# Kernel tuning notes

Measured on AMD Instinct MI355X. Metric: run time of the kernel, lower is better.

Reference implementation:

```python
import jax, jax.numpy as jnp
import numpy as np

B, T, D, H, E, K = 4, 2048, 1024, 2048, 8, 2
LN_EPS = 1e-5


def setup_inputs() -> dict:
    key = jax.random.key(0)
    ks = jax.random.split(key, 5)
    sc = 0.02  # init scale for weights
    return {
        "x": jax.random.normal(ks[0], (B, T, D), dtype=jnp.float32),
        "gate_W": jax.random.normal(ks[1], (D, E), dtype=jnp.float32) * sc,
        "gate_b": jnp.zeros((E,), dtype=jnp.float32),
        "W1": jax.random.normal(ks[2], (E, D, H), dtype=jnp.float32) * sc,
        "b1": jnp.zeros((E, H), dtype=jnp.float32),
        "W2": jax.random.normal(ks[3], (E, H, D), dtype=jnp.float32) * sc,
        "b2": jnp.zeros((E, D), dtype=jnp.float32),
        "ln_gamma": jnp.ones((D,), dtype=jnp.float32),
        "ln_beta": jnp.zeros((D,), dtype=jnp.float32),
    }


def reference(x, gate_W, gate_b, W1, b1, W2, b2, ln_gamma, ln_beta):
    b, t, d = x.shape
    tokens = x.reshape(b * t, d)                      # [N, D]
    n = tokens.shape[0]

    # --- noisy top-k router (eval mode: no noise) ---
    logits = tokens @ gate_W + gate_b                 # [N, E]
    topk_val, topk_idx = jax.lax.top_k(logits, K)     # [N, K]
    topk_prob = jax.nn.softmax(topk_val, axis=-1)
    gates = jnp.zeros_like(logits).at[jnp.arange(n)[:, None], topk_idx].set(topk_prob)  # [N, E]

    # --- experts: dense-equivalent of gather-MLP-scatter (gates are 0 for unselected) ---
    h = jax.nn.gelu(jnp.einsum('nd,edh->enh', tokens, W1) + b1[:, None, :], approximate=False)  # [E,N,H]
    y = jnp.einsum('enh,ehd->end', h, W2) + b2[:, None, :]                                      # [E,N,D]
    out = jnp.einsum('ne,end->nd', gates, y).reshape(b, t, d)

    # --- residual + layernorm ---
    z = out + x
    mu = jnp.mean(z, axis=-1, keepdims=True)
    var = jnp.var(z, axis=-1, keepdims=True)
    out = (z - mu) * jax.lax.rsqrt(var + LN_EPS) * ln_gamma + ln_beta

    # --- aux losses ---
    route_probs = jax.nn.softmax(logits, axis=-1)     # [N, E]
    importance = route_probs.mean(axis=0)             # [E]
    load = (gates > 0).astype(jnp.float32).mean(axis=0)  # [E]
    balance_loss = E * jnp.sum(importance * load)
    eps = 1e-8
    entropy = -(route_probs * jnp.log(route_probs + eps)).sum(axis=-1).mean()
    utilization_entropy = -(load * jnp.log(load + eps)).sum()
    return out, balance_loss, entropy, utilization_entropy, load, importance
```

## Files before the change

### kernel.cpp

```cpp
#include <hip/hip_runtime.h>
#include <math.h>

#define N_TOK 8192
#define DIM   1024
#define HID   2048
#define NE    8
#define NPAIR (N_TOK * 2)
#define CAPP  (NPAIR + NE * 128)
#define TAIL  (N_TOK * DIM)

typedef __bf16 bf16x8_t __attribute__((ext_vector_type(8)));
typedef float  f32x4_t  __attribute__((ext_vector_type(4)));

__device__ __forceinline__ unsigned short f2bf(float f) {
  union { float f; unsigned u; } v; v.f = f;
  unsigned r = v.u + 0x7fffu + ((v.u >> 16) & 1u);
  return (unsigned short)(r >> 16);
}

__device__ __forceinline__ float bf2f(unsigned short h) {
  union { unsigned u; float f; } v; v.u = ((unsigned)h) << 16;
  return v.f;
}

__device__ __forceinline__ float gelu_exact(float v) {
  return 0.5f * v * (1.f + erff(v * 0.70710678118654752440f));
}

__device__ __forceinline__ void load16_lds(const void* g, void* l) {
  __builtin_amdgcn_global_load_lds(
      (const __attribute__((address_space(1))) unsigned int*)g,
      (__attribute__((address_space(3))) unsigned int*)l, 16, 0, 0);
}


template<int KD, int RR>
__global__ __launch_bounds__(256) void w_to_frag(const float* __restrict__ src,
                                                 unsigned short* __restrict__ dst) {
  constexpr int KD32 = KD / 32;
  int z = blockIdx.z;
  int cl = blockIdx.x * 4 + (threadIdx.x >> 6);
  int lane = threadIdx.x & 63, m16 = lane & 15, q = lane >> 4;
  int rblk = cl / KD32, kblk = cl % KD32;
  int r = rblk * 16 + m16;
  int kb = kblk * 32 + q * 8;
  const float* s = src + (size_t)z * KD * RR + (size_t)kb * RR + r;
  unsigned short t[8];
  #pragma unroll
  for (int j = 0; j < 8; ++j) t[j] = f2bf(s[(size_t)j * RR]);
  *(uint4*)(dst + (size_t)z * KD * RR + (size_t)cl * 512 + lane * 8) = *(uint4*)t;
}

#define R_BLOCKS 128
#define R_TPW    (N_TOK / (R_BLOCKS * 4))
__global__ __launch_bounds__(256) void router_kernel(
    const float* __restrict__ x, const float* __restrict__ gW, const float* __restrict__ gb,
    int* __restrict__ tok_e, float* __restrict__ tok_g,
    int* __restrict__ cnt, float* __restrict__ imp, float* __restrict__ ent_sum) {
  __shared__ int s_cnt[NE];
  __shared__ float s_imp[NE];
  __shared__ float s_ent;
  int tid = threadIdx.x;
  if (tid < NE) { s_cnt[tid] = 0; s_imp[tid] = 0.f; }
  if (tid == 0) s_ent = 0.f;
  __syncthreads();
  int wid = tid >> 6, lane = tid & 63;
  int t0 = (blockIdx.x * 4 + wid) * R_TPW;
  float imp_loc[8] = {0.f, 0.f, 0.f, 0.f, 0.f, 0.f, 0.f, 0.f};
  float ent_loc = 0.f;
  for (int t = 0; t < R_TPW; ++t) {
    int n = t0 + t;
    const float* xr = x + (size_t)n * DIM;
    float p[8] = {0.f, 0.f, 0.f, 0.f, 0.f, 0.f, 0.f, 0.f};
    #pragma unroll
    for (int it = 0; it < DIM / 64; ++it) {
      int d = lane + (it << 6);
      float xv = xr[d];
      const float4* g4 = (const float4*)(gW + (size_t)d * NE);
      float4 a = g4[0], b = g4[1];
      p[0] += xv * a.x; p[1] += xv * a.y; p[2] += xv * a.z; p[3] += xv * a.w;
      p[4] += xv * b.x; p[5] += xv * b.y; p[6] += xv * b.z; p[7] += xv * b.w;
    }
    #pragma unroll
    for (int e = 0; e < 8; ++e)
      for (int o = 32; o > 0; o >>= 1) p[e] += __shfl_down(p[e], o, 64);
    if (lane == 0) {
      float lg[8];
      #pragma unroll
      for (int e = 0; e < 8; ++e) lg[e] = p[e] + gb[e];
      int i0 = 0;
      #pragma unroll
      for (int e = 1; e < 8; ++e) if (lg[e] > lg[i0]) i0 = e;
      int i1 = (i0 == 0) ? 1 : 0;
      #pragma unroll
      for (int e = 0; e < 8; ++e) if (e != i0 && lg[e] > lg[i1]) i1 = e;
      float d1 = expf(lg[i1] - lg[i0]);
      float g0 = 1.f / (1.f + d1);
      float g1 = d1 * g0;
      tok_e[2 * n] = i0; tok_e[2 * n + 1] = i1;
      tok_g[2 * n] = g0; tok_g[2 * n + 1] = g1;
      atomicAdd(&s_cnt[i0], 1);
      atomicAdd(&s_cnt[i1], 1);
      float mx = lg[i0], s = 0.f, pe[8];
      #pragma unroll
      for (int e = 0; e < 8; ++e) { pe[e] = expf(lg[e] - mx); s += pe[e]; }
      float inv = 1.f / s;
      #pragma unroll
      for (int e = 0; e < 8; ++e) {
        float pr = pe[e] * inv;
        imp_loc[e] += pr;
        ent_loc -= pr * logf(pr + 1e-8f);
      }
    }
  }
  if (lane == 0) {
    #pragma unroll
    for (int e = 0; e < 8; ++e) atomicAdd(&s_imp[e], imp_loc[e]);
    atomicAdd(&s_ent, ent_loc);
  }
  __syncthreads();
  const float invN = 1.f / (float)N_TOK;
  if (tid < NE) {
    atomicAdd(&cnt[tid], s_cnt[tid]);
    atomicAdd(&imp[tid], s_imp[tid] * invN);
  }
  if (tid == NE) atomicAdd(ent_sum, s_ent * invN);
}

__global__ void finalize_kernel(const int* __restrict__ cnt, int* __restrict__ poffs,
                                int* __restrict__ cursor, const float* __restrict__ imp,
                                const float* __restrict__ ent_sum, float* __restrict__ out_tail) {
  if (threadIdx.x == 0) {
    int off = 0; float bal = 0.f, util = 0.f;
    for (int e = 0; e < NE; ++e) {
      poffs[e] = off; cursor[e] = off;
      off += ((cnt[e] + 127) >> 7) << 7;
      float ld = (float)cnt[e] * (1.f / (float)N_TOK);
      float im = imp[e];
      out_tail[3 + e] = ld;
      out_tail[11 + e] = im;
      bal += im * ld;
      util -= ld * logf(ld + 1e-8f);
    }
    poffs[NE] = off;
    out_tail[0] = (float)NE * bal;
    out_tail[1] = *ent_sum;
    out_tail[2] = util;
  }
}

__global__ __launch_bounds__(256) void scatter_kernel(
    const int* __restrict__ tok_e, const float* __restrict__ tok_g,
    int* __restrict__ cursor, int* __restrict__ row_token, float* __restrict__ row_gate,
    int* __restrict__ pair_slot) {
  __shared__ int s_cnt[NE], s_base[NE], s_rank[NE];
  int tid = threadIdx.x;
  if (tid < NE) { s_cnt[tid] = 0; s_rank[tid] = 0; }
  __syncthreads();
  int n = blockIdx.x * 256 + tid;
  int e0 = tok_e[2 * n], e1 = tok_e[2 * n + 1];
  atomicAdd(&s_cnt[e0], 1);
  atomicAdd(&s_cnt[e1], 1);
  __syncthreads();
  if (tid < NE) s_base[tid] = atomicAdd(&cursor[tid], s_cnt[tid]);
  __syncthreads();
  int r0 = atomicAdd(&s_rank[e0], 1);
  int s0 = s_base[e0] + r0;
  row_token[s0] = n; row_gate[s0] = tok_g[2 * n]; pair_slot[2 * n] = s0;
  int r1 = atomicAdd(&s_rank[e1], 1);
  int s1 = s_base[e1] + r1;
  row_token[s1] = n; row_gate[s1] = tok_g[2 * n + 1]; pair_slot[2 * n + 1] = s1;
}

__global__ __launch_bounds__(256) void gather_a1(
    const float* __restrict__ x, const int* __restrict__ row_token,
    const int* __restrict__ cnt, const int* __restrict__ poffs,
    unsigned short* __restrict__ Ab1) {
  int e = blockIdx.z;
  int base = poffs[e];
  int pcnt = poffs[e + 1] - base;
  int nch = (pcnt >> 4) * 32;
  int cl = blockIdx.x * 4 + (threadIdx.x >> 6);
  if (cl >= nch) return;
  int lane = threadIdx.x & 63, m16 = lane & 15, q = lane >> 4;
  int rblk = cl >> 5, kblk = cl & 31;
  int sl = rblk * 16 + m16;
  int slot = base + sl;
  int tok = (sl < cnt[e]) ? row_token[slot] : 0;
  int k = kblk * 32 + q * 8;
  const float4* sp = (const float4*)(x + (size_t)tok * DIM + k);
  float4 v0 = sp[0], v1 = sp[1];
  unsigned short t[8] = {f2bf(v0.x), f2bf(v0.y), f2bf(v0.z), f2bf(v0.w),
                         f2bf(v1.x), f2bf(v1.y), f2bf(v1.z), f2bf(v1.w)};
  *(uint4*)(Ab1 + ((size_t)(slot >> 4) * 32 + kblk) * 512 + lane * 8) = *(uint4*)t;
}

__global__ __launch_bounds__(256, 4) void expert_gemm1(
    const unsigned short* __restrict__ Ab1,
    const unsigned short* __restrict__ W1f,
    const float* __restrict__ b1,
    const int* __restrict__ poffs,
    unsigned short* __restrict__ He) {
  __shared__ __align__(16) unsigned short As[8192], Bs[8192];
  int e = blockIdx.z;
  int base = poffs[e];
  int pcnt = poffs[e + 1] - base;
  int row0 = blockIdx.x * 128;
  if (row0 >= pcnt) return;
  int col0 = blockIdx.y * 128;
  int tid = threadIdx.x, wid = tid >> 6, lane = tid & 63;
  int m16 = lane & 15, q = lane >> 4;
  int wr = (wid & 1) << 6, wc = (wid >> 1) << 6;
  const unsigned short* Ag = Ab1 + ((size_t)(((base + row0) >> 4) + wid * 2) * 32) * 512 + lane * 8;
  const unsigned short* Bg = W1f + (size_t)e * HID * DIM
                           + ((size_t)((col0 >> 4) + wid * 2) * 32) * 512 + lane * 8;
  unsigned short* lA = As + wid * 4 * 512;
  unsigned short* lB = Bs + wid * 4 * 512;
  f32x4_t zero4 = {0.f, 0.f, 0.f, 0.f};
  f32x4_t acc[4][4];
  #pragma unroll
  for (int i = 0; i < 4; ++i)
    #pragma unroll
    for (int j = 0; j < 4; ++j) acc[i][j] = zero4;
  int ra = wr >> 4, rc = wc >> 4;
  for (int k0 = 0; k0 < DIM; k0 += 64) {
    int kc = (k0 >> 5) * 512;
    load16_lds(Ag + kc,                  lA);
    load16_lds(Ag + kc + 512,            lA + 512);
    load16_lds(Ag + kc + 32 * 512,       lA + 1024);
    load16_lds(Ag + kc + 32 * 512 + 512, lA + 1536);
    load16_lds(Bg + kc,                  lB);
    load16_lds(Bg + kc + 512,            lB + 512);
    load16_lds(Bg + kc + 32 * 512,       lB + 1024);
    load16_lds(Bg + kc + 32 * 512 + 512, lB + 1536);
    __syncthreads();
    #pragma unroll
    for (int ks = 0; ks < 2; ++ks) {
      bf16x8_t a[4], b[4];
      #pragma unroll
      for (int i = 0; i < 4; ++i) {
        a[i] = *(const bf16x8_t*)&As[((ra + i) * 2 + ks) * 512 + lane * 8];
        b[i] = *(const bf16x8_t*)&Bs[((rc + i) * 2 + ks) * 512 + lane * 8];
      }
      #pragma unroll
      for (int i = 0; i < 4; ++i)
        #pragma unroll
        for (int j = 0; j < 4; ++j)
          acc[i][j] = __builtin_amdgcn_mfma_f32_16x16x32_bf16(a[i], b[j], acc[i][j], 0, 0, 0);
    }
    __syncthreads();
  }
  const float* b1e = b1 + (size_t)e * HID;
  int sb = (base + row0) >> 4;
  #pragma unroll
  for (int i = 0; i < 4; ++i) {
    size_t sblk = (size_t)(sb + ra + i);
    #pragma unroll
    for (int rr = 0; rr < 4; ++rr) {
      int s15 = q * 4 + rr;
      #pragma unroll
      for (int j = 0; j < 4; ++j) {
        int col = col0 + wc + j * 16 + m16;
        float v = acc[i][j][rr] + b1e[col];
        size_t off = (sblk * 64 + (col >> 5)) * 512 + (((col >> 3) & 3) * 16 + s15) * 8 + (col & 7);
        He[off] = f2bf(gelu_exact(v));
      }
    }
  }
}

__global__ __launch_bounds__(256, 4) void expert_gemm2(
    const unsigned short* __restrict__ He,
    const unsigned short* __restrict__ W2f,
    const int* __restrict__ poffs,
    unsigned short* __restrict__ yb) {
  __shared__ __align__(16) unsigned short As[8192], Bs[8192];
  int e = blockIdx.z;
  int base = poffs[e];
  int pcnt = poffs[e + 1] - base;
  int row0 = blockIdx.x * 128;
  if (row0 >= pcnt) return;
  int col0 = blockIdx.y * 128;
  int tid = threadIdx.x, wid = tid >> 6, lane = tid & 63;
  int m16 = lane & 15, q = lane >> 4;
  int wr = (wid & 1) << 6, wc = (wid >> 1) << 6;
  const unsigned short* Ag = He + ((size_t)(((base + row0) >> 4) + wid * 2) * 64) * 512 + lane * 8;
  const unsigned short* Bg = W2f + (size_t)e * DIM * HID
                           + ((size_t)((col0 >> 4) + wid * 2) * 64) * 512 + lane * 8;
  unsigned short* lA = As + wid * 4 * 512;
  unsigned short* lB = Bs + wid * 4 * 512;
  f32x4_t zero4 = {0.f, 0.f, 0.f, 0.f};
  f32x4_t acc[4][4];
  #pragma unroll
  for (int i = 0; i < 4; ++i)
    #pragma unroll
    for (int j = 0; j < 4; ++j) acc[i][j] = zero4;
  int ra = wr >> 4, rc = wc >> 4;
  for (int k0 = 0; k0 < HID; k0 += 64) {
    int kc = (k0 >> 5) * 512;
    load16_lds(Ag + kc,                  lA);
    load16_lds(Ag + kc + 512,            lA + 512);
    load16_lds(Ag + kc + 64 * 512,       lA + 1024);
    load16_lds(Ag + kc + 64 * 512 + 512, lA + 1536);
    load16_lds(Bg + kc,                  lB);
    load16_lds(Bg + kc + 512,            lB + 512);
    load16_lds(Bg + kc + 64 * 512,       lB + 1024);
    load16_lds(Bg + kc + 64 * 512 + 512, lB + 1536);
    __syncthreads();
    #pragma unroll
    for (int ks = 0; ks < 2; ++ks) {
      bf16x8_t a[4], b[4];
      #pragma unroll
      for (int i = 0; i < 4; ++i) {
        a[i] = *(const bf16x8_t*)&As[((ra + i) * 2 + ks) * 512 + lane * 8];
        b[i] = *(const bf16x8_t*)&Bs[((rc + i) * 2 + ks) * 512 + lane * 8];
      }
      #pragma unroll
      for (int i = 0; i < 4; ++i)
        #pragma unroll
        for (int j = 0; j < 4; ++j)
          acc[i][j] = __builtin_amdgcn_mfma_f32_16x16x32_bf16(a[i], b[j], acc[i][j], 0, 0, 0);
    }
    __syncthreads();
  }
  #pragma unroll
  for (int i = 0; i < 4; ++i) {
    #pragma unroll
    for (int rr = 0; rr < 4; ++rr) {
      size_t slot = (size_t)(base + row0 + wr + i * 16 + q * 4 + rr);
      #pragma unroll
      for (int j = 0; j < 4; ++j) {
        int col = col0 + wc + j * 16 + m16;
        yb[slot * DIM + col] = f2bf(acc[i][j][rr]);
      }
    }
  }
}

__global__ __launch_bounds__(256) void ln_kernel(
    const float* __restrict__ x, const unsigned short* __restrict__ yb,
    const int* __restrict__ tok_e, const float* __restrict__ tok_g,
    const int* __restrict__ pair_slot, const float* __restrict__ b2,
    const float* __restrict__ gamma, const float* __restrict__ beta,
    float* __restrict__ out) {
  int n = blockIdx.x, tid = threadIdx.x;
  int e0 = tok_e[2 * n], e1 = tok_e[2 * n + 1];
  float g0 = tok_g[2 * n], g1 = tok_g[2 * n + 1];
  size_t s0 = (size_t)pair_slot[2 * n], s1 = (size_t)pair_slot[2 * n + 1];
  const float* xr = x + (size_t)n * DIM;
  const unsigned short* y0 = yb + s0 * DIM;
  const unsigned short* y1 = yb + s1 * DIM;
  const float* b2e0 = b2 + (size_t)e0 * DIM;
  const float* b2e1 = b2 + (size_t)e1 * DIM;
  float z[4], s = 0.f, s2 = 0.f;
  #pragma unroll
  for (int jj = 0; jj < 4; ++jj) {
    int d = tid + (jj << 8);
    float v = xr[d] + g0 * (bf2f(y0[d]) + b2e0[d]) + g1 * (bf2f(y1[d]) + b2e1[d]);
    z[jj] = v; s += v; s2 += v * v;
  }
  for (int o = 32; o > 0; o >>= 1) { s += __shfl_down(s, o, 64); s2 += __shfl_down(s2, o, 64); }
  __shared__ float rs[4], rs2[4];
  int wid = tid >> 6, lane = tid & 63;
  if (lane == 0) { rs[wid] = s; rs2[wid] = s2; }
  __syncthreads();
  float ts = rs[0] + rs[1] + rs[2] + rs[3];
  float ts2 = rs2[0] + rs2[1] + rs2[2] + rs2[3];
  float mu = ts * (1.f / DIM);
  float var = ts2 * (1.f / DIM) - mu * mu;
  float rstd = rsqrtf(var + 1e-5f);
  float* orow = out + (size_t)n * DIM;
  #pragma unroll
  for (int jj = 0; jj < 4; ++jj) {
    int d = tid + (jj << 8);
    orow[d] = (z[jj] - mu) * rstd * gamma[d] + beta[d];
  }
}

extern "C" void kernel_launch(void* const* d_in, const int* in_sizes, int n_in,
                              void* d_out, int out_size, void* d_ws, size_t ws_size,
                              hipStream_t stream) {
  const float* x     = (const float*)d_in[0];
  const float* gW    = (const float*)d_in[1];
  const float* gb    = (const float*)d_in[2];
  const float* W1    = (const float*)d_in[3];
  const float* b1    = (const float*)d_in[4];
  const float* W2    = (const float*)d_in[5];
  const float* b2    = (const float*)d_in[6];
  const float* gamma = (const float*)d_in[7];
  const float* beta  = (const float*)d_in[8];
  float* out = (float*)d_out;

  char* w = (char*)d_ws;
  unsigned short* W1f = (unsigned short*)w; w += (size_t)NE * HID * DIM * 2;
  unsigned short* W2f = (unsigned short*)w; w += (size_t)NE * DIM * HID * 2;
  unsigned short* He  = (unsigned short*)w; w += (size_t)CAPP * HID * 2;
  unsigned short* AbY = (unsigned short*)w; w += (size_t)CAPP * DIM * 2;
  int*   row_token    = (int*)w;            w += (size_t)CAPP * 4;
  float* row_gate     = (float*)w;          w += (size_t)CAPP * 4;
  int*   tok_e        = (int*)w;            w += (size_t)NPAIR * 4;
  float* tok_g        = (float*)w;          w += (size_t)NPAIR * 4;
  int*   pair_slot    = (int*)w;            w += (size_t)NPAIR * 4;
  float* imp          = (float*)w;
  float* ent_sum      = imp + 8;
  int*   cntp         = (int*)(imp + 16);
  int*   cursor       = cntp + 8;
  int*   poffs        = cursor + 8;

  unsigned short* Ab1 = AbY;
  unsigned short* yb  = AbY;

  hipMemsetAsync(imp, 0, 256, stream);

  w_to_frag<DIM, HID><<<dim3(1024, 1, NE), 256, 0, stream>>>(W1, W1f);
  w_to_frag<HID, DIM><<<dim3(1024, 1, NE), 256, 0, stream>>>(W2, W2f);
  router_kernel<<<R_BLOCKS, 256, 0, stream>>>(x, gW, gb, tok_e, tok_g, cntp, imp, ent_sum);
  finalize_kernel<<<1, 64, 0, stream>>>(cntp, poffs, cursor, imp, ent_sum, out + TAIL);
  scatter_kernel<<<N_TOK / 256, 256, 0, stream>>>(tok_e, tok_g, cursor, row_token, row_gate, pair_slot);
  gather_a1<<<dim3(4096, 1, NE), 256, 0, stream>>>(x, row_token, cntp, poffs, Ab1);
  expert_gemm1<<<dim3(64, HID / 128, NE), 256, 0, stream>>>(Ab1, W1f, b1, poffs, He);
  expert_gemm2<<<dim3(64, DIM / 128, NE), 256, 0, stream>>>(He, W2f, poffs, yb);
  ln_kernel<<<N_TOK, 256, 0, stream>>>(x, yb, tok_e, tok_g, pair_slot, b2, gamma, beta, out);
}
```

Measured before the change: 523.0 us.

## Use persistent work-queue tiles in expert GEMMs, fast erf GELU, staged He stores

Both expert GEMMs become persistent kernels that pull tiles from an atomic work counter, using per-expert tile prefix offsets computed in finalize. This avoids launching mostly-empty blocks for the worst-case grid of 64 row tiles per expert. The GEMM1 epilogue now stages GELU output through LDS and writes 16-byte vector stores into He. Exact erf is replaced by the Abramowitz–Stegun polynomial approximation with __expf, which adds a small accuracy error. The router block count is also raised.

```diff
diff --git a/kernel.cpp b/kernel.cpp
--- a/kernel.cpp
+++ b/kernel.cpp
@@ -23,8 +23,15 @@
   return v.f;
 }
 
-__device__ __forceinline__ float gelu_exact(float v) {
-  return 0.5f * v * (1.f + erff(v * 0.70710678118654752440f));
+__device__ __forceinline__ float gelu_fast(float v) {
+  float u = v * 0.70710678118654752440f;
+  float z = fabsf(u);
+  float t = 1.f / (1.f + 0.3275911f * z);
+  float poly = t * (0.254829592f + t * (-0.284496736f + t * (1.421413741f +
+               t * (-1.453152027f + t * 1.061405429f))));
+  float er = 1.f - poly * __expf(-z * z);
+  er = (u < 0.f) ? -er : er;
+  return 0.5f * v * (1.f + er);
 }
 
 __device__ __forceinline__ void load16_lds(const void* g, void* l) {
@@ -51,7 +58,7 @@
   *(uint4*)(dst + (size_t)z * KD * RR + (size_t)cl * 512 + lane * 8) = *(uint4*)t;
 }
 
-#define R_BLOCKS 128
+#define R_BLOCKS 512
 #define R_TPW    (N_TOK / (R_BLOCKS * 4))
 __global__ __launch_bounds__(256) void router_kernel(
     const float* __restrict__ x, const float* __restrict__ gW, const float* __restrict__ gb,
@@ -128,13 +135,18 @@
 }
 
 __global__ void finalize_kernel(const int* __restrict__ cnt, int* __restrict__ poffs,
-                                int* __restrict__ cursor, const float* __restrict__ imp,
+                                int* __restrict__ cursor, int* __restrict__ tb1,
+                                int* __restrict__ tb2, const float* __restrict__ imp,
                                 const float* __restrict__ ent_sum, float* __restrict__ out_tail) {
   if (threadIdx.x == 0) {
-    int off = 0; float bal = 0.f, util = 0.f;
+    int off = 0, t1 = 0, t2 = 0; float bal = 0.f, util = 0.f;
     for (int e = 0; e < NE; ++e) {
-      poffs[e] = off; cursor[e] = off;
-      off += ((cnt[e] + 127) >> 7) << 7;
+      poffs[e] = off; cursor[e] = off; tb1[e] = t1; tb2[e] = t2;
+      int pc = ((cnt[e] + 127) >> 7) << 7;
+      off += pc;
+      int nt = pc >> 7;
+      t1 += nt * (HID / 128);
+      t2 += nt * (DIM / 128);
       float ld = (float)cnt[e] * (1.f / (float)N_TOK);
       float im = imp[e];
       out_tail[3 + e] = ld;
@@ -142,7 +154,7 @@
       bal += im * ld;
       util -= ld * logf(ld + 1e-8f);
     }
-    poffs[NE] = off;
+    poffs[NE] = off; tb1[NE] = t1; tb2[NE] = t2;
     out_tail[0] = (float)NE * bal;
     out_tail[1] = *ent_sum;
     out_tail[2] = util;
@@ -199,141 +211,173 @@
     const unsigned short* __restrict__ Ab1,
     const unsigned short* __restrict__ W1f,
     const float* __restrict__ b1,
-    const int* __restrict__ poffs,
+    const int* __restrict__ poffs, const int* __restrict__ tb1,
+    int* __restrict__ wq,
     unsigned short* __restrict__ He) {
-  __shared__ __align__(16) unsigned short As[8192], Bs[8192];
-  int e = blockIdx.z;
-  int base = poffs[e];
-  int pcnt = poffs[e + 1] - base;
-  int row0 = blockIdx.x * 128;
-  if (row0 >= pcnt) return;
-  int col0 = blockIdx.y * 128;
-  int tid = threadIdx.x, wid = tid >> 6, lane = tid & 63;
+  __shared__ __align__(16) unsigned short Sm[16384];
+  __shared__ int s_tb[NE + 1], s_po[NE + 1], s_t;
+  int tid = threadIdx.x;
+  if (tid <= NE) { s_tb[tid] = tb1[tid]; s_po[tid] = poffs[tid]; }
+  int wid = tid >> 6, lane = tid & 63;
   int m16 = lane & 15, q = lane >> 4;
   int wr = (wid & 1) << 6, wc = (wid >> 1) << 6;
-  const unsigned short* Ag = Ab1 + ((size_t)(((base + row0) >> 4) + wid * 2) * 32) * 512 + lane * 8;
-  const unsigned short* Bg = W1f + (size_t)e * HID * DIM
-                           + ((size_t)((col0 >> 4) + wid * 2) * 32) * 512 + lane * 8;
-  unsigned short* lA = As + wid * 4 * 512;
-  unsigned short* lB = Bs + wid * 4 * 512;
-  f32x4_t zero4 = {0.f, 0.f, 0.f, 0.f};
-  f32x4_t acc[4][4];
-  #pragma unroll
-  for (int i = 0; i < 4; ++i)
-    #pragma unroll
-    for (int j = 0; j < 4; ++j) acc[i][j] = zero4;
   int ra = wr >> 4, rc = wc >> 4;
-  for (int k0 = 0; k0 < DIM; k0 += 64) {
-    int kc = (k0 >> 5) * 512;
-    load16_lds(Ag + kc,                  lA);
-    load16_lds(Ag + kc + 512,            lA + 512);
-    load16_lds(Ag + kc + 32 * 512,       lA + 1024);
-    load16_lds(Ag + kc + 32 * 512 + 512, lA + 1536);
-    load16_lds(Bg + kc,                  lB);
-    load16_lds(Bg + kc + 512,            lB + 512);
-    load16_lds(Bg + kc + 32 * 512,       lB + 1024);
-    load16_lds(Bg + kc + 32 * 512 + 512, lB + 1536);
+  unsigned short* As = Sm;
+  unsigned short* Bs = Sm + 8192;
+  unsigned short* lA = As + wid * 2048;
+  unsigned short* lB = Bs + wid * 2048;
+  unsigned short* Rg = Sm + wid * 4096;
+  for (;;) {
+    if (tid == 0) s_t = atomicAdd(wq, 1);
     __syncthreads();
-    #pragma unroll
-    for (int ks = 0; ks < 2; ++ks) {
-      bf16x8_t a[4], b[4];
-      #pragma unroll
-      for (int i = 0; i < 4; ++i) {
-        a[i] = *(const bf16x8_t*)&As[((ra + i) * 2 + ks) * 512 + lane * 8];
-        b[i] = *(const bf16x8_t*)&Bs[((rc + i) * 2 + ks) * 512 + lane * 8];
+    int t = s_t;
+    if (t >= s_tb[NE]) break;
+    int e = 0;
+    #pragma unroll
+    for (int k = 1; k < NE; ++k) e += (t >= s_tb[k]);
+    int lt = t - s_tb[e];
+    int rt = lt >> 4, ct = lt & 15;
+    int base = s_po[e];
+    int row0 = rt * 128, col0 = ct * 128;
+    const unsigned short* Ag = Ab1 + ((size_t)(((base + row0) >> 4) + wid * 2) * 32) * 512 + lane * 8;
+    const unsigned short* Bg = W1f + (size_t)e * (HID * DIM)
+                             + ((size_t)((col0 >> 4) + wid * 2) * 32) * 512 + lane * 8;
+    f32x4_t zero4 = {0.f, 0.f, 0.f, 0.f};
+    f32x4_t acc[4][4];
+    #pragma unroll
+    for (int i = 0; i < 4; ++i)
+      #pragma unroll
+      for (int j = 0; j < 4; ++j) acc[i][j] = zero4;
+    for (int k0 = 0; k0 < DIM; k0 += 64) {
+      int kc = (k0 >> 5) * 512;
+      load16_lds(Ag + kc,                  lA);
+      load16_lds(Ag + kc + 512,            lA + 512);
+      load16_lds(Ag + kc + 32 * 512,       lA + 1024);
+      load16_lds(Ag + kc + 32 * 512 + 512, lA + 1536);
+      load16_lds(Bg + kc,                  lB);
+      load16_lds(Bg + kc + 512,            lB + 512);
+      load16_lds(Bg + kc + 32 * 512,       lB + 1024);
+      load16_lds(Bg + kc + 32 * 512 + 512, lB + 1536);
+      __syncthreads();
+      #pragma unroll
+      for (int ks = 0; ks < 2; ++ks) {
+        bf16x8_t a[4], b[4];
+        #pragma unroll
+        for (int i = 0; i < 4; ++i) {
+          a[i] = *(const bf16x8_t*)&As[((ra + i) * 2 + ks) * 512 + lane * 8];
+          b[i] = *(const bf16x8_t*)&Bs[((rc + i) * 2 + ks) * 512 + lane * 8];
+        }
+        #pragma unroll
+        for (int i = 0; i < 4; ++i)
+          #pragma unroll
+          for (int j = 0; j < 4; ++j)
+            acc[i][j] = __builtin_amdgcn_mfma_f32_16x16x32_bf16(a[i], b[j], acc[i][j], 0, 0, 0);
       }
-      #pragma unroll
-      for (int i = 0; i < 4; ++i)
-        #pragma unroll
-        for (int j = 0; j < 4; ++j)
-          acc[i][j] = __builtin_amdgcn_mfma_f32_16x16x32_bf16(a[i], b[j], acc[i][j], 0, 0, 0);
+      __syncthreads();
+    }
+    const float* b1e = b1 + (size_t)e * HID;
+    float b1v[4];
+    #pragma unroll
+    for (int j = 0; j < 4; ++j) b1v[j] = b1e[col0 + wc + j * 16 + m16];
+    #pragma unroll
+    for (int i = 0; i < 4; ++i)
+      #pragma unroll
+      for (int j = 0; j < 4; ++j)
+        #pragma unroll
+        for (int rr = 0; rr < 4; ++rr) {
+          float v = acc[i][j][rr] + b1v[j];
+          Rg[(i * 2 + (j >> 1)) * 512 +
+             (((j & 1) * 2 + (m16 >> 3)) * 16 + q * 4 + rr) * 8 + (m16 & 7)] = f2bf(gelu_fast(v));
+        }
+    int sb0 = ((base + row0) >> 4) + ra;
+    int kg0 = (col0 >> 5) + (wc >> 5);
+    #pragma unroll
+    for (int c = 0; c < 8; ++c) {
+      size_t go = ((size_t)(sb0 + (c >> 1)) * 64 + kg0 + (c & 1)) * 512 + lane * 8;
+      *(uint4*)(He + go) = *(uint4*)&Rg[c * 512 + lane * 8];
     }
     __syncthreads();
-  }
-  const float* b1e = b1 + (size_t)e * HID;
-  int sb = (base + row0) >> 4;
-  #pragma unroll
-  for (int i = 0; i < 4; ++i) {
-    size_t sblk = (size_t)(sb + ra + i);
-    #pragma unroll
-    for (int rr = 0; rr < 4; ++rr) {
-      int s15 = q * 4 + rr;
-      #pragma unroll
-      for (int j = 0; j < 4; ++j) {
-        int col = col0 + wc + j * 16 + m16;
-        float v = acc[i][j][rr] + b1e[col];
-        size_t off = (sblk * 64 + (col >> 5)) * 512 + (((col >> 3) & 3) * 16 + s15) * 8 + (col & 7);
-        He[off] = f2bf(gelu_exact(v));
-      }
-    }
   }
 }
 
 __global__ __launch_bounds__(256, 4) void expert_gemm2(
     const unsigned short* __restrict__ He,
     const unsigned short* __restrict__ W2f,
-    const int* __restrict__ poffs,
+    const int* __restrict__ poffs, const int* __restrict__ tb2,
+    int* __restrict__ wq,
     unsigned short* __restrict__ yb) {
-  __shared__ __align__(16) unsigned short As[8192], Bs[8192];
-  int e = blockIdx.z;
-  int base = poffs[e];
-  int pcnt = poffs[e + 1] - base;
-  int row0 = blockIdx.x * 128;
-  if (row0 >= pcnt) return;
-  int col0 = blockIdx.y * 128;
-  int tid = threadIdx.x, wid = tid >> 6, lane = tid & 63;
+  __shared__ __align__(16) unsigned short Sm[16384];
+  __shared__ int s_tb[NE + 1], s_po[NE + 1], s_t;
+  int tid = threadIdx.x;
+  if (tid <= NE) { s_tb[tid] = tb2[tid]; s_po[tid] = poffs[tid]; }
+  int wid = tid >> 6, lane = tid & 63;
   int m16 = lane & 15, q = lane >> 4;
   int wr = (wid & 1) << 6, wc = (wid >> 1) << 6;
-  const unsigned short* Ag = He + ((size_t)(((base + row0) >> 4) + wid * 2) * 64) * 512 + lane * 8;
-  const unsigned short* Bg = W2f + (size_t)e * DIM * HID
-                           + ((size_t)((col0 >> 4) + wid * 2) * 64) * 512 + lane * 8;
-  unsigned short* lA = As + wid * 4 * 512;
-  unsigned short* lB = Bs + wid * 4 * 512;
-  f32x4_t zero4 = {0.f, 0.f, 0.f, 0.f};
-  f32x4_t acc[4][4];
-  #pragma unroll
-  for (int i = 0; i < 4; ++i)
-    #pragma unroll
-    for (int j = 0; j < 4; ++j) acc[i][j] = zero4;
   int ra = wr >> 4, rc = wc >> 4;
-  for (int k0 = 0; k0 < HID; k0 += 64) {
-    int kc = (k0 >> 5) * 512;
-    load16_lds(Ag + kc,                  lA);
-    load16_lds(Ag + kc + 512,            lA + 512);
-    load16_lds(Ag + kc + 64 * 512,       lA + 1024);
-    load16_lds(Ag + kc + 64 * 512 + 512, lA + 1536);
-    load16_lds(Bg + kc,                  lB);
-    load16_lds(Bg + kc + 512,            lB + 512);
-    load16_lds(Bg + kc + 64 * 512,       lB + 1024);
-    load16_lds(Bg + kc + 64 * 512 + 512, lB + 1536);
+  unsigned short* As = Sm;
+  unsigned short* Bs = Sm + 8192;
+  unsigned short* lA = As + wid * 2048;
+  unsigned short* lB = Bs + wid * 2048;
+  for (;;) {
+    if (tid == 0) s_t = atomicAdd(wq, 1);
     __syncthreads();
-    #pragma unroll
-    for (int ks = 0; ks < 2; ++ks) {
-      bf16x8_t a[4], b[4];
-      #pragma unroll
-      for (int i = 0; i < 4; ++i) {
-        a[i] = *(const bf16x8_t*)&As[((ra + i) * 2 + ks) * 512 + lane * 8];
-        b[i] = *(const bf16x8_t*)&Bs[((rc + i) * 2 + ks) * 512 + lane * 8];
+    int t = s_t;
+    if (t >= s_tb[NE]) break;
+    int e = 0;
+    #pragma unroll
+    for (int k = 1; k < NE; ++k) e += (t >= s_tb[k]);
+    int lt = t - s_tb[e];
+    int rt = lt >> 3, ct = lt & 7;
+    int base = s_po[e];
+    int row0 = rt * 128, col0 = ct * 128;
+    const unsigned short* Ag = He + ((size_t)(((base + row0) >> 4) + wid * 2) * 64) * 512 + lane * 8;
+    const unsigned short* Bg = W2f + (size_t)e * (DIM * HID)
+                             + ((size_t)((col0 >> 4) + wid * 2) * 64) * 512 + lane * 8;
+    f32x4_t zero4 = {0.f, 0.f, 0.f, 0.f};
+    f32x4_t acc[4][4];
+    #pragma unroll
+    for (int i = 0; i < 4; ++i)
+      #pragma unroll
+      for (int j = 0; j < 4; ++j) acc[i][j] = zero4;
+    for (int k0 = 0; k0 < HID; k0 += 64) {
+      int kc = (k0 >> 5) * 512;
+      load16_lds(Ag + kc,                  lA);
+      load16_lds(Ag + kc + 512,            lA + 512);
+      load16_lds(Ag + kc + 64 * 512,       lA + 1024);
+      load16_lds(Ag + kc + 64 * 512 + 512, lA + 1536);
+      load16_lds(Bg + kc,                  lB);
+      load16_lds(Bg + kc + 512,            lB + 512);
+      load16_lds(Bg + kc + 64 * 512,       lB + 1024);
+      load16_lds(Bg + kc + 64 * 512 + 512, lB + 1536);
+      __syncthreads();
+      #pragma unroll
+      for (int ks = 0; ks < 2; ++ks) {
+        bf16x8_t a[4], b[4];
+        #pragma unroll
+        for (int i = 0; i < 4; ++i) {
+          a[i] = *(const bf16x8_t*)&As[((ra + i) * 2 + ks) * 512 + lane * 8];
+          b[i] = *(const bf16x8_t*)&Bs[((rc + i) * 2 + ks) * 512 + lane * 8];
+        }
+        #pragma unroll
+        for (int i = 0; i < 4; ++i)
+          #pragma unroll
+          for (int j = 0; j < 4; ++j)
+            acc[i][j] = __builtin_amdgcn_mfma_f32_16x16x32_bf16(a[i], b[j], acc[i][j], 0, 0, 0);
       }
-      #pragma unroll
-      for (int i = 0; i < 4; ++i)
-        #pragma unroll
-        for (int j = 0; j < 4; ++j)
-          acc[i][j] = __builtin_amdgcn_mfma_f32_16x16x32_bf16(a[i], b[j], acc[i][j], 0, 0, 0);
-    }
+      __syncthreads();
+    }
+    #pragma unroll
+    for (int i = 0; i < 4; ++i)
+      #pragma unroll
+      for (int rr = 0; rr < 4; ++rr) {
+        size_t slot = (size_t)(base + row0 + wr + i * 16 + q * 4 + rr);
+        #pragma unroll
+        for (int j = 0; j < 4; ++j) {
+          int col = col0 + wc + j * 16 + m16;
+          yb[slot * DIM + col] = f2bf(acc[i][j][rr]);
+        }
+      }
     __syncthreads();
-  }
-  #pragma unroll
-  for (int i = 0; i < 4; ++i) {
-    #pragma unroll
-    for (int rr = 0; rr < 4; ++rr) {
-      size_t slot = (size_t)(base + row0 + wr + i * 16 + q * 4 + rr);
-      #pragma unroll
-      for (int j = 0; j < 4; ++j) {
-        int col = col0 + wc + j * 16 + m16;
-        yb[slot * DIM + col] = f2bf(acc[i][j][rr]);
-      }
-    }
   }
 }
 
@@ -403,22 +447,26 @@
   int*   pair_slot    = (int*)w;            w += (size_t)NPAIR * 4;
   float* imp          = (float*)w;
   float* ent_sum      = imp + 8;
+  int*   wq1          = (int*)(imp + 9);
+  int*   wq2          = (int*)(imp + 10);
   int*   cntp         = (int*)(imp + 16);
   int*   cursor       = cntp + 8;
   int*   poffs        = cursor + 8;
+  int*   tb1          = poffs + 9;
+  int*   tb2          = tb1 + 9;
 
   unsigned short* Ab1 = AbY;
   unsigned short* yb  = AbY;
 
-  hipMemsetAsync(imp, 0, 256, stream);
+  hipMemsetAsync(imp, 0, 512, stream);
 
   w_to_frag<DIM, HID><<<dim3(1024, 1, NE), 256, 0, stream>>>(W1, W1f);
   w_to_frag<HID, DIM><<<dim3(1024, 1, NE), 256, 0, stream>>>(W2, W2f);
   router_kernel<<<R_BLOCKS, 256, 0, stream>>>(x, gW, gb, tok_e, tok_g, cntp, imp, ent_sum);
-  finalize_kernel<<<1, 64, 0, stream>>>(cntp, poffs, cursor, imp, ent_sum, out + TAIL);
+  finalize_kernel<<<1, 64, 0, stream>>>(cntp, poffs, cursor, tb1, tb2, imp, ent_sum, out + TAIL);
   scatter_kernel<<<N_TOK / 256, 256, 0, stream>>>(tok_e, tok_g, cursor, row_token, row_gate, pair_slot);
   gather_a1<<<dim3(4096, 1, NE), 256, 0, stream>>>(x, row_token, cntp, poffs, Ab1);
-  expert_gemm1<<<dim3(64, HID / 128, NE), 256, 0, stream>>>(Ab1, W1f, b1, poffs, He);
-  expert_gemm2<<<dim3(64, DIM / 128, NE), 256, 0, stream>>>(He, W2f, poffs, yb);
+  expert_gemm1<<<1024, 256, 0, stream>>>(Ab1, W1f, b1, poffs, tb1, wq1, He);
+  expert_gemm2<<<1024, 256, 0, stream>>>(He, W2f, poffs, tb2, wq2, yb);
   ln_kernel<<<N_TOK, 256, 0, stream>>>(x, yb, tok_e, tok_g, pair_slot, b2, gamma, beta, out);
 }
```

New measurement: 563.4 us. 1.08x slower.
